# Kernel tuning notes

Hardware: AMD Instinct MI355X
Metric: run time of the kernel (lower is better)

The kernel has to match this reference:

```python
import jax, jax.numpy as jnp
import numpy as np
import math

B, S, E, H = 8, 1024, 512, 8
EPS = 1e-5

def _ln(x, g, b):
    mu = jnp.mean(x, axis=-1, keepdims=True)
    var = jnp.mean(jnp.square(x - mu), axis=-1, keepdims=True)
    return (x - mu) * jax.lax.rsqrt(var + EPS) * g + b

def setup_inputs() -> dict:
    key = jax.random.key(0)
    ks = iter(jax.random.split(key, 40))
    def w(shape, scale=0.02):
        return jax.random.normal(next(ks), shape, dtype=jnp.float32) * scale
    inp = {
        'x': jax.random.normal(next(ks), (B, S, E), dtype=jnp.float32),
        'cond': jax.random.normal(next(ks), (B, 1, E), dtype=jnp.float32),
        # AdaLN modulation linears (stored as (in,out))
        'g1w': w((E, E)), 'g1b': jnp.zeros((E,), jnp.float32),
        'be1w': w((E, E)), 'be1b': jnp.zeros((E,), jnp.float32),
        'a1w': w((E, E)), 'a1b': jnp.zeros((E,), jnp.float32),
        'g2w': w((E, E)), 'g2b': jnp.zeros((E,), jnp.float32),
        'be2w': w((E, E)), 'be2b': jnp.zeros((E,), jnp.float32),
        'a2w': w((E, E)), 'a2b': jnp.zeros((E,), jnp.float32),
        # LayerNorm affine
        'ln1g': jnp.ones((E,), jnp.float32), 'ln1b': jnp.zeros((E,), jnp.float32),
        'ln2g': jnp.ones((E,), jnp.float32), 'ln2b': jnp.zeros((E,), jnp.float32),
        # attention projections: each head has width E -> out dim H*E
        'wq': w((E, H * E)), 'bq': jnp.zeros((H * E,), jnp.float32),
        'wk': w((E, H * E)), 'bk': jnp.zeros((H * E,), jnp.float32),
        'wv': w((E, H * E)), 'bv': jnp.zeros((H * E,), jnp.float32),
        'lvw': w((H * E, E)), 'lvb': jnp.zeros((E,), jnp.float32),
        # FFN
        'f1w': w((E, 4 * E)), 'f1b': jnp.zeros((4 * E,), jnp.float32),
        'f2w': w((4 * E, E)), 'f2b': jnp.zeros((E,), jnp.float32),
    }
    return inp

def reference(x, cond, g1w, g1b, be1w, be1b, a1w, a1b, g2w, g2b, be2w, be2b, a2w, a2b,
              ln1g, ln1b, ln2g, ln2b, wq, bq, wk, bk, wv, bv, lvw, lvb, f1w, f1b, f2w, f2b):
    # AdaLN modulation signals, each (B,1,E)
    gamma1 = cond @ g1w + g1b
    beta1 = cond @ be1w + be1b
    alpha1 = cond @ a1w + a1b
    gamma2 = cond @ g2w + g2b
    beta2 = cond @ be2w + be2b
    alpha2 = cond @ a2w + a2b

    y = _ln(x, ln1g, ln1b) * (1.0 + gamma1) + beta1
    q = (y @ wq + bq).reshape(B, S, H, E).transpose(0, 2, 1, 3)  # (B,H,S,E)
    k = (y @ wk + bk).reshape(B, S, H, E).transpose(0, 2, 1, 3)
    v = (y @ wv + bv).reshape(B, S, H, E).transpose(0, 2, 1, 3)
    # NOTE: original scales by sqrt(q.size(2)) == sqrt(seq_len), not head_dim
    scale = 1.0 / math.sqrt(S)
    attn = jax.nn.softmax(jnp.einsum('bhse,bhte->bhst', q, k) * scale, axis=-1)
    o = jnp.einsum('bhst,bhte->bhse', attn, v)  # (B,H,S,E)
    o = o.transpose(0, 2, 1, 3).reshape(B, S, H * E)
    y = x + (o @ lvw + lvb) * alpha1

    z = _ln(y, ln2g, ln2b) * (1.0 + gamma2) + beta2
    z = (jax.nn.relu(z @ f1w + f1b) @ f2w + f2b) * alpha2
    return y + z
```

## Files before the change

### kernel.cpp

```cpp
#include <hip/hip_runtime.h>
#include <hip/hip_bf16.h>

typedef __bf16 bf16_t;
typedef bf16_t bf16x8 __attribute__((ext_vector_type(8)));
typedef bf16_t bf16x4 __attribute__((ext_vector_type(4)));
typedef float f32x4 __attribute__((ext_vector_type(4)));

typedef const __attribute__((address_space(1))) void GV;
typedef __attribute__((address_space(3))) void LV;

__device__ __forceinline__ void gload_lds16(const bf16_t* gsrc, bf16_t* ldst) {
    __builtin_amdgcn_global_load_lds((GV*)gsrc, (LV*)ldst, 16, 0, 0);
}

__global__ __launch_bounds__(256) void wtrans_kernel(const float* __restrict__ in,
                                                     bf16_t* __restrict__ out, int K, int N)
{
    __shared__ float tile[32][33];
    const int n0 = blockIdx.x * 32, k0 = blockIdx.y * 32;
    const int tx = threadIdx.x & 31, ty = threadIdx.x >> 5;
#pragma unroll
    for (int i = 0; i < 32; i += 8)
        tile[ty + i][tx] = in[(long long)(k0 + ty + i) * N + n0 + tx];
    __syncthreads();
#pragma unroll
    for (int i = 0; i < 32; i += 8)
        out[(long long)(n0 + ty + i) * K + k0 + tx] = (bf16_t)tile[tx][ty + i];
}

__global__ __launch_bounds__(256) void modsig_kernel(
    const float* __restrict__ cond,
    const float* __restrict__ w0, const float* __restrict__ w1, const float* __restrict__ w2,
    const float* __restrict__ w3, const float* __restrict__ w4, const float* __restrict__ w5,
    const float* __restrict__ c0, const float* __restrict__ c1, const float* __restrict__ c2,
    const float* __restrict__ c3, const float* __restrict__ c4, const float* __restrict__ c5,
    float* __restrict__ out)
{
    __shared__ float cs[512];
    const int sig = blockIdx.x >> 3, b = blockIdx.x & 7;
    const float* w; const float* bi;
    switch (sig) {
        case 0: w = w0; bi = c0; break;
        case 1: w = w1; bi = c1; break;
        case 2: w = w2; bi = c2; break;
        case 3: w = w3; bi = c3; break;
        case 4: w = w4; bi = c4; break;
        default: w = w5; bi = c5; break;
    }
    for (int i = threadIdx.x; i < 512; i += 256) cs[i] = cond[b * 512 + i];
    __syncthreads();
    for (int n = threadIdx.x; n < 512; n += 256) {
        float s = bi[n];
        for (int i = 0; i < 512; ++i) s = fmaf(cs[i], w[(long long)i * 512 + n], s);
        out[(long long)(sig * 8 + b) * 512 + n] = s;
    }
}

__global__ __launch_bounds__(128) void ln_mod_kernel(
    const float* __restrict__ x, const float* __restrict__ g, const float* __restrict__ be,
    const float* __restrict__ gamma, const float* __restrict__ beta, bf16_t* __restrict__ out)
{
    const int row = blockIdx.x;
    const int b = row >> 10;
    const int t = threadIdx.x;
    const float4 v = reinterpret_cast<const float4*>(x + (long long)row * 512)[t];
    float s = v.x + v.y + v.z + v.w;
    float ss = v.x * v.x + v.y * v.y + v.z * v.z + v.w * v.w;
    for (int o = 32; o; o >>= 1) { s += __shfl_xor(s, o); ss += __shfl_xor(ss, o); }
    __shared__ float red[4];
    if ((t & 63) == 0) { red[t >> 6] = s; red[2 + (t >> 6)] = ss; }
    __syncthreads();
    s = red[0] + red[1]; ss = red[2] + red[3];
    const float mu = s * (1.f / 512.f);
    const float rstd = rsqrtf(ss * (1.f / 512.f) - mu * mu + 1e-5f);
    const float4 gv = reinterpret_cast<const float4*>(g)[t];
    const float4 bv = reinterpret_cast<const float4*>(be)[t];
    const float4 ga = reinterpret_cast<const float4*>(gamma + b * 512)[t];
    const float4 bb = reinterpret_cast<const float4*>(beta + b * 512)[t];
    bf16x4 ov;
    ov[0] = (bf16_t)(((v.x - mu) * rstd * gv.x + bv.x) * (1.f + ga.x) + bb.x);
    ov[1] = (bf16_t)(((v.y - mu) * rstd * gv.y + bv.y) * (1.f + ga.y) + bb.y);
    ov[2] = (bf16_t)(((v.z - mu) * rstd * gv.z + bv.z) * (1.f + ga.z) + bb.z);
    ov[3] = (bf16_t)(((v.w - mu) * rstd * gv.w + bv.w) * (1.f + ga.w) + bb.w);
    reinterpret_cast<bf16x4*>(out + (long long)row * 512)[t] = ov;
}

template <int EPI>
__global__ __launch_bounds__(256) void gemm128_kernel(
    const bf16_t* __restrict__ A, const bf16_t* __restrict__ B,
    const float* __restrict__ bias, void* Cout,
    int M, int N, int K, int lda, int ldb, int ldc)
{
    const int m0 = blockIdx.y * 128, n0 = blockIdx.x * 128;
    const int tid = threadIdx.x, lane = tid & 63, wid = tid >> 6;
    const int wr = wid >> 1, wc = wid & 1;

    __shared__ bf16_t As[4096];
    __shared__ bf16_t Bs[4096];

    f32x4 acc[4][4];
#pragma unroll
    for (int m = 0; m < 4; ++m)
#pragma unroll
        for (int n = 0; n < 4; ++n) acc[m][n] = (f32x4){0.f, 0.f, 0.f, 0.f};

    const int r0 = wid * 16 + (lane >> 2);
    const int lc = (lane & 3) ^ ((lane >> 2) & 3);
    const long long aOff0 = (long long)(m0 + r0) * lda + lc * 8;
    const long long aOff1 = (long long)(m0 + r0 + 64) * lda + lc * 8;
    const long long bOff0 = (long long)(n0 + r0) * ldb + lc * 8;
    const long long bOff1 = (long long)(n0 + r0 + 64) * ldb + lc * 8;
    bf16_t* aDst0 = As + wid * 512;
    bf16_t* aDst1 = As + 2048 + wid * 512;
    bf16_t* bDst0 = Bs + wid * 512;
    bf16_t* bDst1 = Bs + 2048 + wid * 512;

    const int frow = lane & 15, lg = lane >> 4;
    const int pc = lg ^ (frow & 3);

    for (int kt = 0; kt < K; kt += 32) {
        gload_lds16(A + aOff0 + kt, aDst0);
        gload_lds16(A + aOff1 + kt, aDst1);
        gload_lds16(B + bOff0 + kt, bDst0);
        gload_lds16(B + bOff1 + kt, bDst1);
        __syncthreads();
        bf16x8 af[4], bfv[4];
#pragma unroll
        for (int m = 0; m < 4; ++m)
            af[m] = *reinterpret_cast<const bf16x8*>(As + (wr * 64 + m * 16 + frow) * 32 + pc * 8);
#pragma unroll
        for (int n = 0; n < 4; ++n)
            bfv[n] = *reinterpret_cast<const bf16x8*>(Bs + (wc * 64 + n * 16 + frow) * 32 + pc * 8);
        __builtin_amdgcn_s_setprio(1);
#pragma unroll
        for (int m = 0; m < 4; ++m)
#pragma unroll
            for (int n = 0; n < 4; ++n)
                acc[m][n] = __builtin_amdgcn_mfma_f32_16x16x32_bf16(af[m], bfv[n], acc[m][n], 0, 0, 0);
        __builtin_amdgcn_s_setprio(0);
        __syncthreads();
    }

#pragma unroll
    for (int m = 0; m < 4; ++m) {
        const int gm = m0 + wr * 64 + m * 16 + ((lane >> 4) << 2);
#pragma unroll
        for (int n = 0; n < 4; ++n) {
            const int gn = n0 + wc * 64 + n * 16 + (lane & 15);
            const float bb = bias ? bias[gn] : 0.f;
#pragma unroll
            for (int j = 0; j < 4; ++j) {
                const float v = acc[m][n][j] + bb;
                const int gmj = gm + j;
                if (EPI == 0) {
                    ((bf16_t*)Cout)[(long long)gmj * ldc + gn] = (bf16_t)v;
                } else {
                    ((bf16_t*)Cout)[(long long)gmj * ldc + gn] = (bf16_t)fmaxf(v, 0.f);
                }
            }
        }
    }
}

__global__ __launch_bounds__(256) void gemmqkv_kernel(
    const bf16_t* __restrict__ A, const bf16_t* __restrict__ B,
    const float* __restrict__ bq, const float* __restrict__ bk, const float* __restrict__ bv,
    bf16_t* __restrict__ qkv, bf16_t* __restrict__ vtb)
{
    const int m0 = blockIdx.y * 128, n0 = blockIdx.x * 128;
    const int sec = n0 >> 12;
    const float* bias = (sec == 0) ? bq : ((sec == 1) ? bk : bv);
    const int tid = threadIdx.x, lane = tid & 63, wid = tid >> 6;
    const int wr = wid >> 1, wc = wid & 1;

    __shared__ bf16_t As[4096];
    __shared__ bf16_t Bs[4096];

    f32x4 acc[4][4];
#pragma unroll
    for (int m = 0; m < 4; ++m)
#pragma unroll
        for (int n = 0; n < 4; ++n) acc[m][n] = (f32x4){0.f, 0.f, 0.f, 0.f};

    const int r0 = wid * 16 + (lane >> 2);
    const int lc = (lane & 3) ^ ((lane >> 2) & 3);
    const long long aOff0 = (long long)(m0 + r0) * 512 + lc * 8;
    const long long aOff1 = (long long)(m0 + r0 + 64) * 512 + lc * 8;
    const long long bOff0 = (long long)(n0 + r0) * 512 + lc * 8;
    const long long bOff1 = (long long)(n0 + r0 + 64) * 512 + lc * 8;
    bf16_t* aDst0 = As + wid * 512;
    bf16_t* aDst1 = As + 2048 + wid * 512;
    bf16_t* bDst0 = Bs + wid * 512;
    bf16_t* bDst1 = Bs + 2048 + wid * 512;

    const int frow = lane & 15, lg = lane >> 4;
    const int pc = lg ^ (frow & 3);

    for (int kt = 0; kt < 512; kt += 32) {
        gload_lds16(A + aOff0 + kt, aDst0);
        gload_lds16(A + aOff1 + kt, aDst1);
        gload_lds16(B + bOff0 + kt, bDst0);
        gload_lds16(B + bOff1 + kt, bDst1);
        __syncthreads();
        bf16x8 af[4], bfv[4];
#pragma unroll
        for (int m = 0; m < 4; ++m)
            af[m] = *reinterpret_cast<const bf16x8*>(As + (wr * 64 + m * 16 + frow) * 32 + pc * 8);
#pragma unroll
        for (int n = 0; n < 4; ++n)
            bfv[n] = *reinterpret_cast<const bf16x8*>(Bs + (wc * 64 + n * 16 + frow) * 32 + pc * 8);
        __builtin_amdgcn_s_setprio(1);
#pragma unroll
        for (int m = 0; m < 4; ++m)
#pragma unroll
            for (int n = 0; n < 4; ++n)
                acc[m][n] = __builtin_amdgcn_mfma_f32_16x16x32_bf16(af[m], bfv[n], acc[m][n], 0, 0, 0);
        __builtin_amdgcn_s_setprio(0);
        __syncthreads();
    }

#pragma unroll
    for (int m = 0; m < 4; ++m) {
        const int gm = m0 + wr * 64 + m * 16 + ((lane >> 4) << 2);
#pragma unroll
        for (int n = 0; n < 4; ++n) {
            const int gn = n0 + wc * 64 + n * 16 + (lane & 15);
            const int gnl = gn & 4095;
            const float bb = bias[gnl];
#pragma unroll
            for (int j = 0; j < 4; ++j) {
                const float v = acc[m][n][j] + bb;
                const int gmj = gm + j;
                if (sec < 2) {
                    qkv[(long long)sec * 33554432 + (long long)gmj * 4096 + gnl] = (bf16_t)v;
                } else {
                    const long long ci =
                        (long long)(((gmj >> 10) * 8 + (gnl >> 9)) * 512 + (gnl & 511)) * 1024 + (gmj & 1023);
                    vtb[ci] = (bf16_t)v;
                }
            }
        }
    }
}

__global__ __launch_bounds__(256) void gemm64_kernel(
    const bf16_t* __restrict__ A, const bf16_t* __restrict__ B,
    const float* __restrict__ bias, float* __restrict__ Cout,
    const float* __restrict__ resid, const float* __restrict__ alpha,
    int M, int N, int K, int lda, int ldb)
{
    const int m0 = blockIdx.y * 64, n0 = blockIdx.x * 128;
    const int tid = threadIdx.x, lane = tid & 63, wid = tid >> 6;
    const int wr = wid >> 1, wc = wid & 1;

    __shared__ bf16_t As[2048];
    __shared__ bf16_t Bs[4096];

    f32x4 acc[2][4];
#pragma unroll
    for (int m = 0; m < 2; ++m)
#pragma unroll
        for (int n = 0; n < 4; ++n) acc[m][n] = (f32x4){0.f, 0.f, 0.f, 0.f};

    const int r0 = wid * 16 + (lane >> 2);
    const int lc = (lane & 3) ^ ((lane >> 2) & 3);
    const long long aOff0 = (long long)(m0 + r0) * lda + lc * 8;
    const long long bOff0 = (long long)(n0 + r0) * ldb + lc * 8;
    const long long bOff1 = (long long)(n0 + r0 + 64) * ldb + lc * 8;
    bf16_t* aDst0 = As + wid * 512;
    bf16_t* bDst0 = Bs + wid * 512;
    bf16_t* bDst1 = Bs + 2048 + wid * 512;

    const int frow = lane & 15, lg = lane >> 4;
    const int pc = lg ^ (frow & 3);

    for (int kt = 0; kt < K; kt += 32) {
        gload_lds16(A + aOff0 + kt, aDst0);
        gload_lds16(B + bOff0 + kt, bDst0);
        gload_lds16(B + bOff1 + kt, bDst1);
        __syncthreads();
        bf16x8 af[2], bfv[4];
#pragma unroll
        for (int m = 0; m < 2; ++m)
            af[m] = *reinterpret_cast<const bf16x8*>(As + (wr * 32 + m * 16 + frow) * 32 + pc * 8);
#pragma unroll
        for (int n = 0; n < 4; ++n)
            bfv[n] = *reinterpret_cast<const bf16x8*>(Bs + (wc * 64 + n * 16 + frow) * 32 + pc * 8);
        __builtin_amdgcn_s_setprio(1);
#pragma unroll
        for (int m = 0; m < 2; ++m)
#pragma unroll
            for (int n = 0; n < 4; ++n)
                acc[m][n] = __builtin_amdgcn_mfma_f32_16x16x32_bf16(af[m], bfv[n], acc[m][n], 0, 0, 0);
        __builtin_amdgcn_s_setprio(0);
        __syncthreads();
    }

#pragma unroll
    for (int m = 0; m < 2; ++m) {
        const int gm = m0 + wr * 32 + m * 16 + ((lane >> 4) << 2);
#pragma unroll
        for (int n = 0; n < 4; ++n) {
            const int gn = n0 + wc * 64 + n * 16 + (lane & 15);
            const float bb = bias[gn];
#pragma unroll
            for (int j = 0; j < 4; ++j) {
                const int gmj = gm + j;
                const long long ci = (long long)gmj * 512 + gn;
                Cout[ci] = resid[ci] + (acc[m][n][j] + bb) * alpha[(gmj >> 10) * 512 + gn];
            }
        }
    }
}

#define FA_LDS 75776
#define SCL 0.04508422132207354f
__global__ __launch_bounds__(512, 2) void flash_kernel(
    bf16_t* __restrict__ qb, const bf16_t* __restrict__ kb, const bf16_t* __restrict__ vtb)
{
    extern __shared__ char smem[];
    bf16_t* KVs = (bf16_t*)smem;
    char* PB = smem + 65536;
    float* pmaxB = (float*)(smem + 73728);
    float* psumB = (float*)(smem + 74752);

    const int bid = blockIdx.x;
    const int xcd = bid & 7, idx = bid >> 3;
    const int qt = idx & 15, bhl = idx >> 4;
    const int bh = xcd * 8 + bhl;
    const int b = bh >> 3, h = bh & 7;
    const int q0 = qt * 64;
    const int tid = threadIdx.x, lane = tid & 63, wid = tid >> 6;
    const int laneq = lane & 15, lx = lane & 7, lg = lane >> 4;
    const int wk = wid >> 2, wq = wid & 3;
    const int we = wid & 3, wq2 = wid >> 2;

#pragma unroll
    for (int r = 0; r < 8; ++r) {
        const int row = r * 8 + wid;
        gload_lds16(kb + ((long long)(b * 1024 + row) * 8 + h) * 512 + ((lane ^ (row & 7)) << 3),
                    KVs + row * 512);
    }
    const int qi = wq * 16 + laneq;
    bf16x8 qfrag[16];
    {
        const bf16_t* qrow = qb + ((long long)(b * 1024 + q0 + qi) * 8 + h) * 512 + lg * 8;
#pragma unroll
        for (int ks = 0; ks < 16; ++ks) qfrag[ks] = *reinterpret_cast<const bf16x8*>(qrow + ks * 32);
    }
    f32x4 accA[8], accB[8];
#pragma unroll
    for (int e = 0; e < 8; ++e) { accA[e] = (f32x4){0.f,0.f,0.f,0.f}; accB[e] = (f32x4){0.f,0.f,0.f,0.f}; }
    float mS = 0.f, mPA = 0.f, mPB = 0.f, lA = 0.f, lB = 0.f;
    const int rA0 = wk * 32 + laneq, rA1 = rA0 + 16;
    const int qA = wq2 * 32 + laneq, qB = qA + 16;
    const int qx = (qi & 7) << 1;
    const int qxA = (qA & 7) << 1, qxB = (qB & 7) << 1;

    for (int t = 0; t < 16; ++t) {
        __syncthreads();
        f32x4 s0 = (f32x4){0.f,0.f,0.f,0.f}, s1 = (f32x4){0.f,0.f,0.f,0.f};
        const char* KsB = (const char*)KVs;
        __builtin_amdgcn_s_setprio(1);
#pragma unroll
        for (int ks = 0; ks < 16; ++ks) {
            const int co = ((ks * 4 + lg) ^ lx) << 4;
            bf16x8 a0 = *(const bf16x8*)(KsB + rA0 * 1024 + co);
            bf16x8 a1 = *(const bf16x8*)(KsB + rA1 * 1024 + co);
            s0 = __builtin_amdgcn_mfma_f32_16x16x32_bf16(a0, qfrag[ks], s0, 0, 0, 0);
            s1 = __builtin_amdgcn_mfma_f32_16x16x32_bf16(a1, qfrag[ks], s1, 0, 0, 0);
        }
        __builtin_amdgcn_s_setprio(0);
        float f[8];
#pragma unroll
        for (int j = 0; j < 4; ++j) { f[j] = s0[j] * SCL; f[4 + j] = s1[j] * SCL; }
        float mloc = f[0];
#pragma unroll
        for (int j = 1; j < 8; ++j) mloc = fmaxf(mloc, f[j]);
        mloc = fmaxf(mloc, __shfl_xor(mloc, 16));
        mloc = fmaxf(mloc, __shfl_xor(mloc, 32));
        float pe[8]; float sl = 0.f;
#pragma unroll
        for (int j = 0; j < 8; ++j) { pe[j] = exp2f(f[j] - mS); sl += pe[j]; }
        sl += __shfl_xor(sl, 16);
        sl += __shfl_xor(sl, 32);
        __syncthreads();
#pragma unroll
        for (int r = 0; r < 8; ++r) {
            const int e = r * 64 + wid * 8 + (lane >> 3);
            gload_lds16(vtb + ((long long)bh * 512 + e) * 1024 + t * 64 + ((lx ^ (e & 7)) << 3),
                        KVs + (r * 64 + wid * 8) * 64);
        }
        if (lane < 16) {
            pmaxB[(t & 1) * 128 + wk * 64 + wq * 16 + lane] = mloc;
            psumB[(t & 1) * 128 + wk * 64 + wq * 16 + lane] = sl;
        }
        {
            bf16x4 p0, p1;
#pragma unroll
            for (int j = 0; j < 4; ++j) { p0[j] = (bf16_t)pe[j]; p1[j] = (bf16_t)pe[4 + j]; }
            const int kc0 = wk * 8 + lg, kc1 = kc0 + 4;
            *(bf16x4*)(PB + qi * 128 + ((kc0 ^ qx) << 3)) = p0;
            *(bf16x4*)(PB + qi * 128 + ((kc1 ^ qx) << 3)) = p1;
        }
        __syncthreads();
        const char* VB = (const char*)KVs;
        __builtin_amdgcn_s_setprio(1);
#pragma unroll
        for (int ks2 = 0; ks2 < 2; ++ks2) {
            const int kcp = ks2 * 8 + lg * 2;
            bf16x8 pA = *(const bf16x8*)(PB + qA * 128 + ((kcp ^ qxA) << 3));
            bf16x8 pBv = *(const bf16x8*)(PB + qB * 128 + ((kcp ^ qxB) << 3));
            const int kcv = ks2 * 4 + lg;
#pragma unroll
            for (int ef = 0; ef < 8; ++ef) {
                const int re = we * 128 + ef * 16 + laneq;
                bf16x8 av = *(const bf16x8*)(VB + re * 128 + ((kcv ^ lx) << 4));
                accA[ef] = __builtin_amdgcn_mfma_f32_16x16x32_bf16(av, pA, accA[ef], 0, 0, 0);
                accB[ef] = __builtin_amdgcn_mfma_f32_16x16x32_bf16(av, pBv, accB[ef], 0, 0, 0);
            }
        }
        __builtin_amdgcn_s_setprio(0);
        {
            const float* pmax_t = pmaxB + (t & 1) * 128;
            const float* psum_t = psumB + (t & 1) * 128;
            mS = fmaxf(mS, fmaxf(pmax_t[qi], pmax_t[64 + qi]));
            lA += psum_t[qA] + psum_t[64 + qA];
            lB += psum_t[qB] + psum_t[64 + qB];
            const float mnA = fmaxf(mPA, fmaxf(pmax_t[qA], pmax_t[64 + qA]));
            const float mnB = fmaxf(mPB, fmaxf(pmax_t[qB], pmax_t[64 + qB]));
            if (__ballot((mnA > mPA) || (mnB > mPB))) {
                const float rA = exp2f(mPA - mnA), rB = exp2f(mPB - mnB);
                lA *= rA; lB *= rB;
#pragma unroll
                for (int e = 0; e < 8; ++e) {
#pragma unroll
                    for (int j = 0; j < 4; ++j) { accA[e][j] *= rA; accB[e][j] *= rB; }
                }
            }
            mPA = mnA; mPB = mnB;
        }
        __syncthreads();
        if (t < 15) {
#pragma unroll
            for (int r = 0; r < 8; ++r) {
                const int row = r * 8 + wid;
                gload_lds16(kb + ((long long)(b * 1024 + t * 64 + 64 + row) * 8 + h) * 512
                                + ((lane ^ (row & 7)) << 3),
                            KVs + row * 512);
            }
        }
    }

    const float iA = 1.f / lA, iB = 1.f / lB;
#pragma unroll
    for (int ef = 0; ef < 8; ++ef) {
        const int e0 = we * 128 + ef * 16 + lg * 4;
        bf16x4 oA, oB;
#pragma unroll
        for (int j = 0; j < 4; ++j) { oA[j] = (bf16_t)(accA[ef][j] * iA); oB[j] = (bf16_t)(accB[ef][j] * iB); }
        *(bf16x4*)(qb + ((long long)(b * 1024 + q0 + qA) * 8 + h) * 512 + e0) = oA;
        *(bf16x4*)(qb + ((long long)(b * 1024 + q0 + qB) * 8 + h) * 512 + e0) = oB;
    }
}

extern "C" void kernel_launch(void* const* d_in, const int* in_sizes, int n_in,
                              void* d_out, int out_size, void* d_ws, size_t ws_size,
                              hipStream_t stream)
{
    const float* x    = (const float*)d_in[0];
    const float* cond = (const float*)d_in[1];
    const float* g1w  = (const float*)d_in[2];  const float* g1b  = (const float*)d_in[3];
    const float* be1w = (const float*)d_in[4];  const float* be1b = (const float*)d_in[5];
    const float* a1w  = (const float*)d_in[6];  const float* a1b  = (const float*)d_in[7];
    const float* g2w  = (const float*)d_in[8];  const float* g2b  = (const float*)d_in[9];
    const float* be2w = (const float*)d_in[10]; const float* be2b = (const float*)d_in[11];
    const float* a2w  = (const float*)d_in[12]; const float* a2b  = (const float*)d_in[13];
    const float* ln1g = (const float*)d_in[14]; const float* ln1b = (const float*)d_in[15];
    const float* ln2g = (const float*)d_in[16]; const float* ln2b = (const float*)d_in[17];
    const float* wq   = (const float*)d_in[18]; const float* bq   = (const float*)d_in[19];
    const float* wk   = (const float*)d_in[20]; const float* bk   = (const float*)d_in[21];
    const float* wv   = (const float*)d_in[22]; const float* bv   = (const float*)d_in[23];
    const float* lvw  = (const float*)d_in[24]; const float* lvb  = (const float*)d_in[25];
    const float* f1w  = (const float*)d_in[26]; const float* f1b  = (const float*)d_in[27];
    const float* f2w  = (const float*)d_in[28]; const float* f2b  = (const float*)d_in[29];
    (void)in_sizes; (void)n_in; (void)out_size; (void)ws_size;

    char* w8 = (char*)d_ws;
    float*  mod  = (float*)(w8);
    bf16_t* wqT  = (bf16_t*)(w8 + 98304);
    bf16_t* lvwT = (bf16_t*)(w8 + 98304 + 3 * 4194304);
    bf16_t* f1wT = (bf16_t*)(w8 + 98304 + 4 * 4194304);
    bf16_t* f2wT = (bf16_t*)(w8 + 98304 + 4 * 4194304 + 2097152);
    bf16_t* ybf  = (bf16_t*)(w8 + 98304 + 4 * 4194304 + 2 * 2097152);
    bf16_t* qb   = (bf16_t*)(w8 + 98304 + 4 * 4194304 + 2 * 2097152 + 8388608);
    bf16_t* kb   = qb + 33554432;
    bf16_t* vtb  = kb + 33554432;

    (void)hipFuncSetAttribute((const void*)flash_kernel,
                              hipFuncAttributeMaxDynamicSharedMemorySize, FA_LDS);

    const dim3 blk(256);
    wtrans_kernel<<<dim3(128, 16), blk, 0, stream>>>(wq, wqT, 512, 4096);
    wtrans_kernel<<<dim3(128, 16), blk, 0, stream>>>(wk, wqT + 2097152, 512, 4096);
    wtrans_kernel<<<dim3(128, 16), blk, 0, stream>>>(wv, wqT + 2 * 2097152, 512, 4096);
    wtrans_kernel<<<dim3(16, 128), blk, 0, stream>>>(lvw, lvwT, 4096, 512);
    wtrans_kernel<<<dim3(64, 16), blk, 0, stream>>>(f1w, f1wT, 512, 2048);
    wtrans_kernel<<<dim3(16, 64), blk, 0, stream>>>(f2w, f2wT, 2048, 512);
    modsig_kernel<<<48, blk, 0, stream>>>(cond, g1w, be1w, a1w, g2w, be2w, a2w,
                                          g1b, be1b, a1b, g2b, be2b, a2b, mod);
    ln_mod_kernel<<<8192, 128, 0, stream>>>(x, ln1g, ln1b, mod, mod + 4096, ybf);
    gemmqkv_kernel<<<dim3(96, 64), blk, 0, stream>>>(ybf, wqT, bq, bk, bv, qb, vtb);
    flash_kernel<<<1024, 512, FA_LDS, stream>>>(qb, kb, vtb);
    gemm64_kernel<<<dim3(4, 128), blk, 0, stream>>>(qb, lvwT, lvb, (float*)d_out, x, mod + 8192,
        8192, 512, 4096, 4096, 4096);
    ln_mod_kernel<<<8192, 128, 0, stream>>>((const float*)d_out, ln2g, ln2b,
                                            mod + 12288, mod + 16384, ybf);
    gemm128_kernel<1><<<dim3(16, 64), blk, 0, stream>>>(ybf, f1wT, f1b, qb,
        8192, 2048, 512, 512, 512, 2048);
    gemm64_kernel<<<dim3(4, 128), blk, 0, stream>>>(qb, f2wT, f2b, (float*)d_out,
        (const float*)d_out, mod + 20480,
        8192, 512, 2048, 2048, 2048);
}
```

Baseline: 748.0 us.

## Double K-depth GEMM tiles, swizzle block order, split flash K/V buffers

Measured after the change: 691.6 us. 1.08x faster.

```diff
diff --git a/kernel.cpp b/kernel.cpp
--- a/kernel.cpp
+++ b/kernel.cpp
@@ -91,12 +91,16 @@
     const float* __restrict__ bias, void* Cout,
     int M, int N, int K, int lda, int ldb, int ldc)
 {
-    const int m0 = blockIdx.y * 128, n0 = blockIdx.x * 128;
+    const int nbx = gridDim.x;
+    const int lin = blockIdx.y * nbx + blockIdx.x;
+    const int cpx = (nbx * gridDim.y) >> 3;
+    const int swz = (lin & 7) * cpx + (lin >> 3);
+    const int m0 = (swz / nbx) * 128, n0 = (swz % nbx) * 128;
     const int tid = threadIdx.x, lane = tid & 63, wid = tid >> 6;
     const int wr = wid >> 1, wc = wid & 1;
 
-    __shared__ bf16_t As[4096];
-    __shared__ bf16_t Bs[4096];
+    __shared__ bf16_t As[8192];
+    __shared__ bf16_t Bs[8192];
 
     f32x4 acc[4][4];
 #pragma unroll
@@ -104,39 +108,42 @@
 #pragma unroll
         for (int n = 0; n < 4; ++n) acc[m][n] = (f32x4){0.f, 0.f, 0.f, 0.f};
 
-    const int r0 = wid * 16 + (lane >> 2);
-    const int lc = (lane & 3) ^ ((lane >> 2) & 3);
-    const long long aOff0 = (long long)(m0 + r0) * lda + lc * 8;
-    const long long aOff1 = (long long)(m0 + r0 + 64) * lda + lc * 8;
-    const long long bOff0 = (long long)(n0 + r0) * ldb + lc * 8;
-    const long long bOff1 = (long long)(n0 + r0 + 64) * ldb + lc * 8;
-    bf16_t* aDst0 = As + wid * 512;
-    bf16_t* aDst1 = As + 2048 + wid * 512;
-    bf16_t* bDst0 = Bs + wid * 512;
-    bf16_t* bDst1 = Bs + 2048 + wid * 512;
+    const int r8 = lane >> 3;
+    const int lc = (lane & 7) ^ r8;
+    long long aOff[4], bOff[4];
+#pragma unroll
+    for (int i = 0; i < 4; ++i) {
+        const int row = i * 32 + wid * 8 + r8;
+        aOff[i] = (long long)(m0 + row) * lda + lc * 8;
+        bOff[i] = (long long)(n0 + row) * ldb + lc * 8;
+    }
 
     const int frow = lane & 15, lg = lane >> 4;
-    const int pc = lg ^ (frow & 3);
-
-    for (int kt = 0; kt < K; kt += 32) {
-        gload_lds16(A + aOff0 + kt, aDst0);
-        gload_lds16(A + aOff1 + kt, aDst1);
-        gload_lds16(B + bOff0 + kt, bDst0);
-        gload_lds16(B + bOff1 + kt, bDst1);
-        __syncthreads();
-        bf16x8 af[4], bfv[4];
-#pragma unroll
-        for (int m = 0; m < 4; ++m)
-            af[m] = *reinterpret_cast<const bf16x8*>(As + (wr * 64 + m * 16 + frow) * 32 + pc * 8);
-#pragma unroll
-        for (int n = 0; n < 4; ++n)
-            bfv[n] = *reinterpret_cast<const bf16x8*>(Bs + (wc * 64 + n * 16 + frow) * 32 + pc * 8);
+    const int p0 = lg ^ (frow & 7);
+
+    for (int kt = 0; kt < K; kt += 64) {
+#pragma unroll
+        for (int i = 0; i < 4; ++i) gload_lds16(A + aOff[i] + kt, As + i * 2048 + wid * 512);
+#pragma unroll
+        for (int i = 0; i < 4; ++i) gload_lds16(B + bOff[i] + kt, Bs + i * 2048 + wid * 512);
+        __syncthreads();
         __builtin_amdgcn_s_setprio(1);
 #pragma unroll
-        for (int m = 0; m < 4; ++m)
+        for (int kk = 0; kk < 2; ++kk) {
+            const int pc = p0 ^ (kk << 2);
+            bf16x8 af[4], bfv[4];
+#pragma unroll
+            for (int m = 0; m < 4; ++m)
+                af[m] = *reinterpret_cast<const bf16x8*>(As + (wr * 64 + m * 16 + frow) * 64 + pc * 8);
 #pragma unroll
             for (int n = 0; n < 4; ++n)
-                acc[m][n] = __builtin_amdgcn_mfma_f32_16x16x32_bf16(af[m], bfv[n], acc[m][n], 0, 0, 0);
+                bfv[n] = *reinterpret_cast<const bf16x8*>(Bs + (wc * 64 + n * 16 + frow) * 64 + pc * 8);
+#pragma unroll
+            for (int m = 0; m < 4; ++m)
+#pragma unroll
+                for (int n = 0; n < 4; ++n)
+                    acc[m][n] = __builtin_amdgcn_mfma_f32_16x16x32_bf16(af[m], bfv[n], acc[m][n], 0, 0, 0);
+        }
         __builtin_amdgcn_s_setprio(0);
         __syncthreads();
     }
@@ -167,14 +174,16 @@
     const float* __restrict__ bq, const float* __restrict__ bk, const float* __restrict__ bv,
     bf16_t* __restrict__ qkv, bf16_t* __restrict__ vtb)
 {
-    const int m0 = blockIdx.y * 128, n0 = blockIdx.x * 128;
+    const int lin = blockIdx.y * 96 + blockIdx.x;
+    const int swz = (lin & 7) * 768 + (lin >> 3);
+    const int m0 = (swz / 96) * 128, n0 = (swz % 96) * 128;
     const int sec = n0 >> 12;
     const float* bias = (sec == 0) ? bq : ((sec == 1) ? bk : bv);
     const int tid = threadIdx.x, lane = tid & 63, wid = tid >> 6;
     const int wr = wid >> 1, wc = wid & 1;
 
-    __shared__ bf16_t As[4096];
-    __shared__ bf16_t Bs[4096];
+    __shared__ bf16_t As[8192];
+    __shared__ bf16_t Bs[8192];
 
     f32x4 acc[4][4];
 #pragma unroll
@@ -182,39 +191,42 @@
 #pragma unroll
         for (int n = 0; n < 4; ++n) acc[m][n] = (f32x4){0.f, 0.f, 0.f, 0.f};
 
-    const int r0 = wid * 16 + (lane >> 2);
-    const int lc = (lane & 3) ^ ((lane >> 2) & 3);
-    const long long aOff0 = (long long)(m0 + r0) * 512 + lc * 8;
-    const long long aOff1 = (long long)(m0 + r0 + 64) * 512 + lc * 8;
-    const long long bOff0 = (long long)(n0 + r0) * 512 + lc * 8;
-    const long long bOff1 = (long long)(n0 + r0 + 64) * 512 + lc * 8;
-    bf16_t* aDst0 = As + wid * 512;
-    bf16_t* aDst1 = As + 2048 + wid * 512;
-    bf16_t* bDst0 = Bs + wid * 512;
-    bf16_t* bDst1 = Bs + 2048 + wid * 512;
+    const int r8 = lane >> 3;
+    const int lc = (lane & 7) ^ r8;
+    long long aOff[4], bOff[4];
+#pragma unroll
+    for (int i = 0; i < 4; ++i) {
+        const int row = i * 32 + wid * 8 + r8;
+        aOff[i] = (long long)(m0 + row) * 512 + lc * 8;
+        bOff[i] = (long long)(n0 + row) * 512 + lc * 8;
+    }
 
     const int frow = lane & 15, lg = lane >> 4;
-    const int pc = lg ^ (frow & 3);
-
-    for (int kt = 0; kt < 512; kt += 32) {
-        gload_lds16(A + aOff0 + kt, aDst0);
-        gload_lds16(A + aOff1 + kt, aDst1);
-        gload_lds16(B + bOff0 + kt, bDst0);
-        gload_lds16(B + bOff1 + kt, bDst1);
-        __syncthreads();
-        bf16x8 af[4], bfv[4];
-#pragma unroll
-        for (int m = 0; m < 4; ++m)
-            af[m] = *reinterpret_cast<const bf16x8*>(As + (wr * 64 + m * 16 + frow) * 32 + pc * 8);
-#pragma unroll
-        for (int n = 0; n < 4; ++n)
-            bfv[n] = *reinterpret_cast<const bf16x8*>(Bs + (wc * 64 + n * 16 + frow) * 32 + pc * 8);
+    const int p0 = lg ^ (frow & 7);
+
+    for (int kt = 0; kt < 512; kt += 64) {
+#pragma unroll
+        for (int i = 0; i < 4; ++i) gload_lds16(A + aOff[i] + kt, As + i * 2048 + wid * 512);
+#pragma unroll
+        for (int i = 0; i < 4; ++i) gload_lds16(B + bOff[i] + kt, Bs + i * 2048 + wid * 512);
+        __syncthreads();
         __builtin_amdgcn_s_setprio(1);
 #pragma unroll
-        for (int m = 0; m < 4; ++m)
+        for (int kk = 0; kk < 2; ++kk) {
+            const int pc = p0 ^ (kk << 2);
+            bf16x8 af[4], bfv[4];
+#pragma unroll
+            for (int m = 0; m < 4; ++m)
+                af[m] = *reinterpret_cast<const bf16x8*>(As + (wr * 64 + m * 16 + frow) * 64 + pc * 8);
 #pragma unroll
             for (int n = 0; n < 4; ++n)
-                acc[m][n] = __builtin_amdgcn_mfma_f32_16x16x32_bf16(af[m], bfv[n], acc[m][n], 0, 0, 0);
+                bfv[n] = *reinterpret_cast<const bf16x8*>(Bs + (wc * 64 + n * 16 + frow) * 64 + pc * 8);
+#pragma unroll
+            for (int m = 0; m < 4; ++m)
+#pragma unroll
+                for (int n = 0; n < 4; ++n)
+                    acc[m][n] = __builtin_amdgcn_mfma_f32_16x16x32_bf16(af[m], bfv[n], acc[m][n], 0, 0, 0);
+        }
         __builtin_amdgcn_s_setprio(0);
         __syncthreads();
     }
@@ -249,12 +261,16 @@
     const float* __restrict__ resid, const float* __restrict__ alpha,
     int M, int N, int K, int lda, int ldb)
 {
-    const int m0 = blockIdx.y * 64, n0 = blockIdx.x * 128;
+    const int nbx = gridDim.x;
+    const int lin = blockIdx.y * nbx + blockIdx.x;
+    const int cpx = (nbx * gridDim.y) >> 3;
+    const int swz = (lin & 7) * cpx + (lin >> 3);
+    const int m0 = (swz / nbx) * 64, n0 = (swz % nbx) * 128;
     const int tid = threadIdx.x, lane = tid & 63, wid = tid >> 6;
     const int wr = wid >> 1, wc = wid & 1;
 
-    __shared__ bf16_t As[2048];
-    __shared__ bf16_t Bs[4096];
+    __shared__ bf16_t As[4096];
+    __shared__ bf16_t Bs[8192];
 
     f32x4 acc[2][4];
 #pragma unroll
@@ -262,36 +278,42 @@
 #pragma unroll
         for (int n = 0; n < 4; ++n) acc[m][n] = (f32x4){0.f, 0.f, 0.f, 0.f};
 
-    const int r0 = wid * 16 + (lane >> 2);
-    const int lc = (lane & 3) ^ ((lane >> 2) & 3);
-    const long long aOff0 = (long long)(m0 + r0) * lda + lc * 8;
-    const long long bOff0 = (long long)(n0 + r0) * ldb + lc * 8;
-    const long long bOff1 = (long long)(n0 + r0 + 64) * ldb + lc * 8;
-    bf16_t* aDst0 = As + wid * 512;
-    bf16_t* bDst0 = Bs + wid * 512;
-    bf16_t* bDst1 = Bs + 2048 + wid * 512;
+    const int r8 = lane >> 3;
+    const int lc = (lane & 7) ^ r8;
+    long long aOff[2], bOff[4];
+#pragma unroll
+    for (int i = 0; i < 2; ++i)
+        aOff[i] = (long long)(m0 + i * 32 + wid * 8 + r8) * lda + lc * 8;
+#pragma unroll
+    for (int i = 0; i < 4; ++i)
+        bOff[i] = (long long)(n0 + i * 32 + wid * 8 + r8) * ldb + lc * 8;
 
     const int frow = lane & 15, lg = lane >> 4;
-    const int pc = lg ^ (frow & 3);
-
-    for (int kt = 0; kt < K; kt += 32) {
-        gload_lds16(A + aOff0 + kt, aDst0);
-        gload_lds16(B + bOff0 + kt, bDst0);
-        gload_lds16(B + bOff1 + kt, bDst1);
-        __syncthreads();
-        bf16x8 af[2], bfv[4];
-#pragma unroll
-        for (int m = 0; m < 2; ++m)
-            af[m] = *reinterpret_cast<const bf16x8*>(As + (wr * 32 + m * 16 + frow) * 32 + pc * 8);
-#pragma unroll
-        for (int n = 0; n < 4; ++n)
-            bfv[n] = *reinterpret_cast<const bf16x8*>(Bs + (wc * 64 + n * 16 + frow) * 32 + pc * 8);
+    const int p0 = lg ^ (frow & 7);
+
+    for (int kt = 0; kt < K; kt += 64) {
+#pragma unroll
+        for (int i = 0; i < 2; ++i) gload_lds16(A + aOff[i] + kt, As + i * 2048 + wid * 512);
+#pragma unroll
+        for (int i = 0; i < 4; ++i) gload_lds16(B + bOff[i] + kt, Bs + i * 2048 + wid * 512);
+        __syncthreads();
         __builtin_amdgcn_s_setprio(1);
 #pragma unroll
-        for (int m = 0; m < 2; ++m)
+        for (int kk = 0; kk < 2; ++kk) {
+            const int pc = p0 ^ (kk << 2);
+            bf16x8 af[2], bfv[4];
+#pragma unroll
+            for (int m = 0; m < 2; ++m)
+                af[m] = *reinterpret_cast<const bf16x8*>(As + (wr * 32 + m * 16 + frow) * 64 + pc * 8);
 #pragma unroll
             for (int n = 0; n < 4; ++n)
-                acc[m][n] = __builtin_amdgcn_mfma_f32_16x16x32_bf16(af[m], bfv[n], acc[m][n], 0, 0, 0);
+                bfv[n] = *reinterpret_cast<const bf16x8*>(Bs + (wc * 64 + n * 16 + frow) * 64 + pc * 8);
+#pragma unroll
+            for (int m = 0; m < 2; ++m)
+#pragma unroll
+                for (int n = 0; n < 4; ++n)
+                    acc[m][n] = __builtin_amdgcn_mfma_f32_16x16x32_bf16(af[m], bfv[n], acc[m][n], 0, 0, 0);
+        }
         __builtin_amdgcn_s_setprio(0);
         __syncthreads();
     }
@@ -313,16 +335,17 @@
     }
 }
 
-#define FA_LDS 75776
+#define FA_LDS 141312
 #define SCL 0.04508422132207354f
 __global__ __launch_bounds__(512, 2) void flash_kernel(
     bf16_t* __restrict__ qb, const bf16_t* __restrict__ kb, const bf16_t* __restrict__ vtb)
 {
     extern __shared__ char smem[];
-    bf16_t* KVs = (bf16_t*)smem;
-    char* PB = smem + 65536;
-    float* pmaxB = (float*)(smem + 73728);
-    float* psumB = (float*)(smem + 74752);
+    bf16_t* Ks = (bf16_t*)smem;
+    bf16_t* Vs = (bf16_t*)(smem + 65536);
+    char* PB = smem + 131072;
+    float* pmaxB = (float*)(smem + 139264);
+    float* psumB = (float*)(smem + 140288);
 
     const int bid = blockIdx.x;
     const int xcd = bid & 7, idx = bid >> 3;
@@ -339,7 +362,7 @@
     for (int r = 0; r < 8; ++r) {
         const int row = r * 8 + wid;
         gload_lds16(kb + ((long long)(b * 1024 + row) * 8 + h) * 512 + ((lane ^ (row & 7)) << 3),
-                    KVs + row * 512);
+                    Ks + row * 512);
     }
     const int qi = wq * 16 + laneq;
     bf16x8 qfrag[16];
@@ -356,11 +379,18 @@
     const int qA = wq2 * 32 + laneq, qB = qA + 16;
     const int qx = (qi & 7) << 1;
     const int qxA = (qA & 7) << 1, qxB = (qB & 7) << 1;
+    __syncthreads();
 
     for (int t = 0; t < 16; ++t) {
-        __syncthreads();
+        const int kv0 = t * 64;
+#pragma unroll
+        for (int r = 0; r < 8; ++r) {
+            const int e = r * 64 + wid * 8 + (lane >> 3);
+            gload_lds16(vtb + ((long long)bh * 512 + e) * 1024 + kv0 + ((lx ^ (e & 7)) << 3),
+                        Vs + (r * 64 + wid * 8) * 64);
+        }
         f32x4 s0 = (f32x4){0.f,0.f,0.f,0.f}, s1 = (f32x4){0.f,0.f,0.f,0.f};
-        const char* KsB = (const char*)KVs;
+        const char* KsB = (const char*)Ks;
         __builtin_amdgcn_s_setprio(1);
 #pragma unroll
         for (int ks = 0; ks < 16; ++ks) {
@@ -384,13 +414,6 @@
         for (int j = 0; j < 8; ++j) { pe[j] = exp2f(f[j] - mS); sl += pe[j]; }
         sl += __shfl_xor(sl, 16);
         sl += __shfl_xor(sl, 32);
-        __syncthreads();
-#pragma unroll
-        for (int r = 0; r < 8; ++r) {
-            const int e = r * 64 + wid * 8 + (lane >> 3);
-            gload_lds16(vtb + ((long long)bh * 512 + e) * 1024 + t * 64 + ((lx ^ (e & 7)) << 3),
-                        KVs + (r * 64 + wid * 8) * 64);
-        }
         if (lane < 16) {
             pmaxB[(t & 1) * 128 + wk * 64 + wq * 16 + lane] = mloc;
             psumB[(t & 1) * 128 + wk * 64 + wq * 16 + lane] = sl;
@@ -404,7 +427,17 @@
             *(bf16x4*)(PB + qi * 128 + ((kc1 ^ qx) << 3)) = p1;
         }
         __syncthreads();
-        const char* VB = (const char*)KVs;
+
+        if (t < 15) {
+#pragma unroll
+            for (int r = 0; r < 8; ++r) {
+                const int row = r * 8 + wid;
+                gload_lds16(kb + ((long long)(b * 1024 + kv0 + 64 + row) * 8 + h) * 512
+                                + ((lane ^ (row & 7)) << 3),
+                            Ks + row * 512);
+            }
+        }
+        const char* VB = (const char*)Vs;
         __builtin_amdgcn_s_setprio(1);
 #pragma unroll
         for (int ks2 = 0; ks2 < 2; ++ks2) {
@@ -441,15 +474,6 @@
             mPA = mnA; mPB = mnB;
         }
         __syncthreads();
-        if (t < 15) {
-#pragma unroll
-            for (int r = 0; r < 8; ++r) {
-                const int row = r * 8 + wid;
-                gload_lds16(kb + ((long long)(b * 1024 + t * 64 + 64 + row) * 8 + h) * 512
-                                + ((lane ^ (row & 7)) << 3),
-                            KVs + row * 512);
-            }
-        }
     }
 
     const float iA = 1.f / lA, iB = 1.f / lB;
```
